# Performance work log

Hardware: AMD Instinct MI355X
Metric: run time of the kernel (lower is better)

## Reference

```python
import jax, jax.numpy as jnp
import numpy as np

NUM_EMBEDDINGS = 8192
EMBEDDING_DIM = 256
PROJECTION_DIM = 128


def setup_inputs() -> dict:
    key = jax.random.key(0)
    k_x, k_cb, k_w, k_b = jax.random.split(key, 4)
    x = jax.random.normal(k_x, (16, 1024, EMBEDDING_DIM), dtype=jnp.float32)
    codebook = jax.random.normal(k_cb, (NUM_EMBEDDINGS, EMBEDDING_DIM), dtype=jnp.float32)
    proj_w = jax.random.normal(k_w, (EMBEDDING_DIM, PROJECTION_DIM), dtype=jnp.float32) / np.sqrt(EMBEDDING_DIM)
    proj_b = jax.random.normal(k_b, (PROJECTION_DIM,), dtype=jnp.float32) * 0.01
    return {"x": x, "codebook": codebook, "proj_w": proj_w, "proj_b": proj_b}


def reference(x, codebook, proj_w, proj_b):
    # Flatten tokens: [N, D]
    x_flat = x.reshape(-1, EMBEDDING_DIM)
    # Project tokens and codebook into the distance space: [N, P], [K, P]
    x_proj = x_flat @ proj_w + proj_b
    cb_proj = codebook @ proj_w + proj_b
    # Squared euclidean distances via expansion: [N, K]
    distances = (
        jnp.sum(x_proj ** 2, axis=1, keepdims=True)
        - 2.0 * (x_proj @ cb_proj.T)
        + jnp.sum(cb_proj ** 2, axis=1)
    )
    idx = jnp.argmin(distances, axis=1)
    discrete = jax.nn.one_hot(idx, NUM_EMBEDDINGS, dtype=x.dtype)  # [N, K]
    # One-hot matmul lookup (disguised gather): [N, D]
    quantized = (discrete @ codebook).reshape(x.shape)
    return (discrete, quantized)
```

## Files before the change

kernel.cpp:

```cpp
#include <hip/hip_runtime.h>
#include <math.h>

#define D 256
#define P 128
#define K 8192
#define NTOK 16384
#define NROWS (NTOK + K)
#define NCHUNK 8
#define KCHUNK (K / NCHUNK)
#define CAPC 128
#define MARGIN 3.0f
#define FLT_BIG 3.402823466e+38f

typedef __attribute__((ext_vector_type(8))) short bf16x8;
typedef __attribute__((ext_vector_type(4))) float f32x4;
typedef __attribute__((ext_vector_type(8))) unsigned short u16x8;

__device__ __forceinline__ unsigned short f32_to_bf16_rne(float f) {
    unsigned int u = __float_as_uint(f);
    u = (u + 0x7fffu + ((u >> 16) & 1u)) >> 16;
    return (unsigned short)u;
}

__global__ __launch_bounds__(256) void proj_kernel(
    const float* __restrict__ x, const float* __restrict__ cb,
    const float* __restrict__ w, const float* __restrict__ bias,
    float* __restrict__ xproj, float* __restrict__ cproj,
    float* __restrict__ xnorm, float* __restrict__ cnorm,
    unsigned short* __restrict__ xh, unsigned short* __restrict__ chs,
    int* __restrict__ cnt)
{
    __shared__ float As[16][D];
    const int tid = threadIdx.x;
    const int row0 = blockIdx.x * 16;

    {
        int g = blockIdx.x * 256 + tid;
        if (g < NTOK) cnt[g] = 0;
    }

    for (int i = tid; i < 16 * (D / 4); i += 256) {
        int r = i / (D / 4);
        int c4 = i % (D / 4);
        int gr = row0 + r;
        const float* src = (gr < NTOK) ? (x + (size_t)gr * D)
                                       : (cb + (size_t)(gr - NTOK) * D);
        float4 v = ((const float4*)src)[c4];
        ((float4*)&As[r][0])[c4] = v;
    }
    __syncthreads();

    const int r = tid >> 4;
    const int c0 = (tid & 15) * 8;

    float acc[8];
#pragma unroll
    for (int j = 0; j < 8; j++) acc[j] = 0.f;

    for (int d = 0; d < D; d += 4) {
        float4 a4 = *(const float4*)&As[r][d];
#pragma unroll
        for (int dd = 0; dd < 4; dd++) {
            float av = (dd == 0) ? a4.x : (dd == 1) ? a4.y : (dd == 2) ? a4.z : a4.w;
            float4 w0 = *(const float4*)&w[(size_t)(d + dd) * P + c0];
            float4 w1 = *(const float4*)&w[(size_t)(d + dd) * P + c0 + 4];
            acc[0] = fmaf(av, w0.x, acc[0]);
            acc[1] = fmaf(av, w0.y, acc[1]);
            acc[2] = fmaf(av, w0.z, acc[2]);
            acc[3] = fmaf(av, w0.w, acc[3]);
            acc[4] = fmaf(av, w1.x, acc[4]);
            acc[5] = fmaf(av, w1.y, acc[5]);
            acc[6] = fmaf(av, w1.z, acc[6]);
            acc[7] = fmaf(av, w1.w, acc[7]);
        }
    }

    float out[8];
    float nrm = 0.f;
    u16x8 hv;
#pragma unroll
    for (int j = 0; j < 8; j++) {
        out[j] = acc[j] + bias[c0 + j];
        nrm = fmaf(out[j], out[j], nrm);
        hv[j] = f32_to_bf16_rne(out[j]);
    }

    const int gr = row0 + r;
    if (gr < NTOK) {
        float* dst = xproj + (size_t)gr * P;
        float4 o0; o0.x = out[0]; o0.y = out[1]; o0.z = out[2]; o0.w = out[3];
        float4 o1; o1.x = out[4]; o1.y = out[5]; o1.z = out[6]; o1.w = out[7];
        *(float4*)&dst[c0] = o0;
        *(float4*)&dst[c0 + 4] = o1;
        *(u16x8*)(xh + (size_t)gr * P + c0) = hv;
    } else {
        int row = gr - NTOK;
        float* dst = cproj + (size_t)row * P;
        float4 o0; o0.x = out[0]; o0.y = out[1]; o0.z = out[2]; o0.w = out[3];
        float4 o1; o1.x = out[4]; o1.y = out[5]; o1.z = out[6]; o1.w = out[7];
        *(float4*)&dst[c0] = o0;
        *(float4*)&dst[c0 + 4] = o1;
        int t64 = row >> 6, rg = (row >> 4) & 3, l15 = row & 15;
        int ks = c0 >> 5, quad = (c0 >> 3) & 3;
        size_t atom = ((size_t)(t64 * 16 + rg * 4 + ks) * 4 + quad) * 16 + l15;
        *(u16x8*)(chs + atom * 8) = hv;
    }

#pragma unroll
    for (int off = 1; off < 16; off <<= 1)
        nrm += __shfl_xor(nrm, off, 16);
    if ((tid & 15) == 0) {
        if (gr < NTOK) xnorm[gr] = nrm;
        else           cnorm[gr - NTOK] = nrm;
    }
}

__global__ __launch_bounds__(256) void filterz_kernel(
    const unsigned short* __restrict__ xh, const unsigned short* __restrict__ chs,
    const float* __restrict__ xnorm, const float* __restrict__ cnorm,
    int* __restrict__ cnt, int* __restrict__ cand,
    float* __restrict__ discrete)
{
    const int tid = threadIdx.x;
    const int tok0 = blockIdx.x * 128;
    const int k0 = blockIdx.y * KCHUNK;
    const int flat = blockIdx.y * gridDim.x + blockIdx.x;

    const int wave = tid >> 6;
    const int lane = tid & 63;
    const int quad = lane >> 4;
    const int l15 = lane & 15;

    f32x4* zbase = (f32x4*)discrete + (size_t)flat * 32768;
    const f32x4 zv = (f32x4)(0.f);

    bf16x8 afrag[2][4];
#pragma unroll
    for (int mi = 0; mi < 2; mi++)
#pragma unroll
        for (int ks = 0; ks < 4; ks++)
            afrag[mi][ks] = *(const bf16x8*)(
                xh + (size_t)(tok0 + wave * 32 + mi * 16 + l15) * P + ks * 32 + quad * 8);

    float xnv[2][4];
#pragma unroll
    for (int mi = 0; mi < 2; mi++)
#pragma unroll
        for (int r = 0; r < 4; r++)
            xnv[mi][r] = xnorm[tok0 + wave * 32 + mi * 16 + quad * 4 + r];

    float rmin[2][4];
#pragma unroll
    for (int mi = 0; mi < 2; mi++)
#pragma unroll
        for (int r = 0; r < 4; r++) rmin[mi][r] = FLT_BIG;

    for (int ct = 0; ct < KCHUNK / 64; ct++) {
        const int kt = k0 + ct * 64;
        const int t64 = kt >> 6;

#pragma unroll
        for (int s = 0; s < 8; s++)
            zbase[(size_t)ct * 2048 + s * 256 + tid] = zv;

        f32x4 acc[2][4];
#pragma unroll
        for (int mi = 0; mi < 2; mi++)
#pragma unroll
            for (int nj = 0; nj < 4; nj++)
                acc[mi][nj] = (f32x4)(0.f);

#pragma unroll
        for (int ks = 0; ks < 4; ks++) {
            const bf16x8* base = (const bf16x8*)(chs) + (size_t)(t64 * 16 + ks) * 64 + lane;
            bf16x8 b0 = base[0 * 4 * 64];
            bf16x8 b1 = base[1 * 4 * 64];
            bf16x8 b2 = base[2 * 4 * 64];
            bf16x8 b3 = base[3 * 4 * 64];
            acc[0][0] = __builtin_amdgcn_mfma_f32_16x16x32_bf16(afrag[0][ks], b0, acc[0][0], 0, 0, 0);
            acc[0][1] = __builtin_amdgcn_mfma_f32_16x16x32_bf16(afrag[0][ks], b1, acc[0][1], 0, 0, 0);
            acc[0][2] = __builtin_amdgcn_mfma_f32_16x16x32_bf16(afrag[0][ks], b2, acc[0][2], 0, 0, 0);
            acc[0][3] = __builtin_amdgcn_mfma_f32_16x16x32_bf16(afrag[0][ks], b3, acc[0][3], 0, 0, 0);
            acc[1][0] = __builtin_amdgcn_mfma_f32_16x16x32_bf16(afrag[1][ks], b0, acc[1][0], 0, 0, 0);
            acc[1][1] = __builtin_amdgcn_mfma_f32_16x16x32_bf16(afrag[1][ks], b1, acc[1][1], 0, 0, 0);
            acc[1][2] = __builtin_amdgcn_mfma_f32_16x16x32_bf16(afrag[1][ks], b2, acc[1][2], 0, 0, 0);
            acc[1][3] = __builtin_amdgcn_mfma_f32_16x16x32_bf16(afrag[1][ks], b3, acc[1][3], 0, 0, 0);
        }

        float cn[4];
#pragma unroll
        for (int nj = 0; nj < 4; nj++) cn[nj] = cnorm[kt + nj * 16 + l15];

#pragma unroll
        for (int mi = 0; mi < 2; mi++)
#pragma unroll
            for (int r = 0; r < 4; r++) {
                float d[4];
#pragma unroll
                for (int nj = 0; nj < 4; nj++)
                    d[nj] = (xnv[mi][r] - 2.0f * acc[mi][nj][r]) + cn[nj];
                float m = fminf(fminf(d[0], d[1]), fminf(d[2], d[3]));
#pragma unroll
                for (int off = 1; off < 16; off <<= 1)
                    m = fminf(m, __shfl_xor(m, off));
                float rm = fminf(rmin[mi][r], m);
                rmin[mi][r] = rm;
                float thr = rm + MARGIN;
                const int tok = tok0 + wave * 32 + mi * 16 + quad * 4 + r;
#pragma unroll
                for (int nj = 0; nj < 4; nj++) {
                    if (d[nj] <= thr) {
                        int pos = atomicAdd(&cnt[tok], 1);
                        if (pos < CAPC) cand[(size_t)tok * CAPC + pos] = kt + nj * 16 + l15;
                    }
                }
            }
    }
}

__global__ __launch_bounds__(256) void rescorefinal_kernel(
    const float* __restrict__ xproj, const float* __restrict__ cproj,
    const float* __restrict__ xnorm, const float* __restrict__ cnorm,
    const int* __restrict__ cnt, const int* __restrict__ cand,
    const float* __restrict__ cb,
    float* __restrict__ discrete, float* __restrict__ quant)
{
    __shared__ int sidx[64];
    const int tid = threadIdx.x;
    const int lane = tid & 63;
    const int wave = tid >> 6;
    const int tok0 = blockIdx.x * 64;

    for (int i = 0; i < 16; i++) {
        const int t = tok0 + wave * 16 + i;
        int n = cnt[t];
        if (n > CAPC) n = CAPC;
        const float xn = xnorm[t];
        const float* xr = xproj + (size_t)t * P;

        unsigned long long pack = 0xFFFFFFFFFFFFFFFFull;
        for (int j = lane; j < n; j += 64) {
            int k = cand[(size_t)t * CAPC + j];
            const float* cr = cproj + (size_t)k * P;
            float s = 0.f;
#pragma unroll 8
            for (int p = 0; p < P; p += 4) {
                float4 a = *(const float4*)&xr[p];
                float4 b = *(const float4*)&cr[p];
                s = fmaf(a.x, b.x, s);
                s = fmaf(a.y, b.y, s);
                s = fmaf(a.z, b.z, s);
                s = fmaf(a.w, b.w, s);
            }
            float dist = (xn - 2.0f * s) + cnorm[k];
            unsigned long long pk =
                ((unsigned long long)__float_as_uint(dist) << 32) |
                (unsigned long long)(unsigned)k;
            if (pk < pack) pack = pk;
        }
#pragma unroll
        for (int off = 1; off < 64; off <<= 1) {
            unsigned long long o = __shfl_xor((long long)pack, off);
            if (o < pack) pack = o;
        }
        if (lane == 0) {
            int bi = (int)(pack & 0xFFFFFFFFull);
            sidx[wave * 16 + i] = bi;
            discrete[(size_t)t * K + bi] = 1.0f;
        }
    }
    __syncthreads();

    for (int i = tid; i < 64 * (D / 4); i += 256) {
        int t = i >> 6;
        int c4 = i & 63;
        int bi = sidx[t];
        float4 v = ((const float4*)(cb + (size_t)bi * D))[c4];
        ((float4*)(quant + (size_t)(tok0 + t) * D))[c4] = v;
    }
}

extern "C" void kernel_launch(void* const* d_in, const int* in_sizes, int n_in,
                              void* d_out, int out_size, void* d_ws, size_t ws_size,
                              hipStream_t stream) {
    const float* x    = (const float*)d_in[0];
    const float* cb   = (const float*)d_in[1];
    const float* w    = (const float*)d_in[2];
    const float* bias = (const float*)d_in[3];

    float* out = (float*)d_out;
    float* discrete = out;
    float* quant = out + (size_t)NTOK * K;

    char* ws = (char*)d_ws;
    size_t off = 0;
    float* xproj = (float*)(ws + off); off += (size_t)NTOK * P * 4;
    float* cproj = (float*)(ws + off); off += (size_t)K * P * 4;
    float* xnorm = (float*)(ws + off); off += (size_t)NTOK * 4;
    float* cnorm = (float*)(ws + off); off += (size_t)K * 4;
    unsigned short* xh  = (unsigned short*)(ws + off); off += (size_t)NTOK * P * 2;
    unsigned short* chs = (unsigned short*)(ws + off); off += (size_t)K * P * 2;
    int* cnt  = (int*)(ws + off); off += (size_t)NTOK * 4;
    int* cand = (int*)(ws + off); off += (size_t)NTOK * CAPC * 4;

    proj_kernel<<<dim3(NROWS / 16), dim3(256), 0, stream>>>(
        x, cb, w, bias, xproj, cproj, xnorm, cnorm, xh, chs, cnt);

    filterz_kernel<<<dim3(NTOK / 128, NCHUNK), dim3(256), 0, stream>>>(
        xh, chs, xnorm, cnorm, cnt, cand, discrete);

    rescorefinal_kernel<<<dim3(NTOK / 64), dim3(256), 0, stream>>>(
        xproj, cproj, xnorm, cnorm, cnt, cand, cb, discrete, quant);
}
```

Before: 895.5 us.

## Fuse projection, filter and rescore into one cooperative persistent kernel

Merges the three kernels into a single cooperative kernel of 512 blocks that uses grid-wide syncs between the projection, the candidate filter and the rescore/gather phases. Zeroing of the large one-hot output moves to the start of the kernel as a grid-stride loop, so it is no longer interleaved with the MFMA filter. The filter is re-tiled so each block handles 64 tokens over half the codebook, and the candidate cap is halved. This removes launch gaps and lets the zero-fill overlap other work, but caps parallelism at 512 blocks, adds grid-sync cost, and risks overflowing the smaller candidate list.

```diff
diff --git a/kernel.cpp b/kernel.cpp
--- a/kernel.cpp
+++ b/kernel.cpp
@@ -1,4 +1,5 @@
 #include <hip/hip_runtime.h>
+#include <hip/hip_cooperative_groups.h>
 #include <math.h>
 
 #define D 256
@@ -6,11 +7,10 @@
 #define K 8192
 #define NTOK 16384
 #define NROWS (NTOK + K)
-#define NCHUNK 8
-#define KCHUNK (K / NCHUNK)
-#define CAPC 128
+#define CAPC 64
 #define MARGIN 3.0f
 #define FLT_BIG 3.402823466e+38f
+#define GRID 512
 
 typedef __attribute__((ext_vector_type(8))) short bf16x8;
 typedef __attribute__((ext_vector_type(4))) float f32x4;
@@ -22,191 +22,175 @@
     return (unsigned short)u;
 }
 
-__global__ __launch_bounds__(256) void proj_kernel(
+__global__ __launch_bounds__(256, 2) void mega_kernel(
     const float* __restrict__ x, const float* __restrict__ cb,
     const float* __restrict__ w, const float* __restrict__ bias,
     float* __restrict__ xproj, float* __restrict__ cproj,
     float* __restrict__ xnorm, float* __restrict__ cnorm,
     unsigned short* __restrict__ xh, unsigned short* __restrict__ chs,
-    int* __restrict__ cnt)
+    int* __restrict__ cnt, int* __restrict__ cand,
+    float* __restrict__ discrete, float* __restrict__ quant)
 {
+    cooperative_groups::grid_group grid = cooperative_groups::this_grid();
+
     __shared__ float As[16][D];
+    __shared__ int sidx[32];
+
     const int tid = threadIdx.x;
-    const int row0 = blockIdx.x * 16;
+    const int bid = blockIdx.x;
+    const int lane = tid & 63;
+    const int wave = tid >> 6;
+    const int quad = lane >> 4;
+    const int l15 = lane & 15;
 
     {
-        int g = blockIdx.x * 256 + tid;
+        f32x4* p = (f32x4*)discrete;
+        const f32x4 zv = (f32x4)(0.f);
+        size_t i = (size_t)bid * 256 + tid;
+        const size_t n4 = (size_t)NTOK * K / 4;
+        for (; i < n4; i += (size_t)GRID * 256) p[i] = zv;
+        int g = bid * 256 + tid;
         if (g < NTOK) cnt[g] = 0;
     }
 
-    for (int i = tid; i < 16 * (D / 4); i += 256) {
-        int r = i / (D / 4);
-        int c4 = i % (D / 4);
-        int gr = row0 + r;
-        const float* src = (gr < NTOK) ? (x + (size_t)gr * D)
-                                       : (cb + (size_t)(gr - NTOK) * D);
-        float4 v = ((const float4*)src)[c4];
-        ((float4*)&As[r][0])[c4] = v;
-    }
-    __syncthreads();
-
-    const int r = tid >> 4;
-    const int c0 = (tid & 15) * 8;
-
-    float acc[8];
-#pragma unroll
-    for (int j = 0; j < 8; j++) acc[j] = 0.f;
-
-    for (int d = 0; d < D; d += 4) {
-        float4 a4 = *(const float4*)&As[r][d];
-#pragma unroll
-        for (int dd = 0; dd < 4; dd++) {
-            float av = (dd == 0) ? a4.x : (dd == 1) ? a4.y : (dd == 2) ? a4.z : a4.w;
-            float4 w0 = *(const float4*)&w[(size_t)(d + dd) * P + c0];
-            float4 w1 = *(const float4*)&w[(size_t)(d + dd) * P + c0 + 4];
-            acc[0] = fmaf(av, w0.x, acc[0]);
-            acc[1] = fmaf(av, w0.y, acc[1]);
-            acc[2] = fmaf(av, w0.z, acc[2]);
-            acc[3] = fmaf(av, w0.w, acc[3]);
-            acc[4] = fmaf(av, w1.x, acc[4]);
-            acc[5] = fmaf(av, w1.y, acc[5]);
-            acc[6] = fmaf(av, w1.z, acc[6]);
-            acc[7] = fmaf(av, w1.w, acc[7]);
-        }
-    }
-
-    float out[8];
-    float nrm = 0.f;
-    u16x8 hv;
-#pragma unroll
-    for (int j = 0; j < 8; j++) {
-        out[j] = acc[j] + bias[c0 + j];
-        nrm = fmaf(out[j], out[j], nrm);
-        hv[j] = f32_to_bf16_rne(out[j]);
-    }
-
-    const int gr = row0 + r;
-    if (gr < NTOK) {
-        float* dst = xproj + (size_t)gr * P;
+    for (int u = bid; u < NROWS / 16; u += GRID) {
+        const int row0 = u * 16;
+        __syncthreads();
+        for (int i = tid; i < 16 * (D / 4); i += 256) {
+            int r = i / (D / 4);
+            int c4 = i % (D / 4);
+            int gr = row0 + r;
+            const float* src = (gr < NTOK) ? (x + (size_t)gr * D)
+                                           : (cb + (size_t)(gr - NTOK) * D);
+            float4 v = ((const float4*)src)[c4];
+            ((float4*)&As[r][0])[c4] = v;
+        }
+        __syncthreads();
+
+        const int r = tid >> 4;
+        const int c0 = (tid & 15) * 8;
+
+        float acc[8];
+#pragma unroll
+        for (int j = 0; j < 8; j++) acc[j] = 0.f;
+
+        for (int d = 0; d < D; d += 4) {
+            float4 a4 = *(const float4*)&As[r][d];
+#pragma unroll
+            for (int dd = 0; dd < 4; dd++) {
+                float av = (dd == 0) ? a4.x : (dd == 1) ? a4.y : (dd == 2) ? a4.z : a4.w;
+                float4 w0 = *(const float4*)&w[(size_t)(d + dd) * P + c0];
+                float4 w1 = *(const float4*)&w[(size_t)(d + dd) * P + c0 + 4];
+                acc[0] = fmaf(av, w0.x, acc[0]);
+                acc[1] = fmaf(av, w0.y, acc[1]);
+                acc[2] = fmaf(av, w0.z, acc[2]);
+                acc[3] = fmaf(av, w0.w, acc[3]);
+                acc[4] = fmaf(av, w1.x, acc[4]);
+                acc[5] = fmaf(av, w1.y, acc[5]);
+                acc[6] = fmaf(av, w1.z, acc[6]);
+                acc[7] = fmaf(av, w1.w, acc[7]);
+            }
+        }
+
+        float out[8];
+        float nrm = 0.f;
+        u16x8 hv;
+#pragma unroll
+        for (int j = 0; j < 8; j++) {
+            out[j] = acc[j] + bias[c0 + j];
+            nrm = fmaf(out[j], out[j], nrm);
+            hv[j] = f32_to_bf16_rne(out[j]);
+        }
+
+        const int gr = row0 + r;
         float4 o0; o0.x = out[0]; o0.y = out[1]; o0.z = out[2]; o0.w = out[3];
         float4 o1; o1.x = out[4]; o1.y = out[5]; o1.z = out[6]; o1.w = out[7];
-        *(float4*)&dst[c0] = o0;
-        *(float4*)&dst[c0 + 4] = o1;
-        *(u16x8*)(xh + (size_t)gr * P + c0) = hv;
-    } else {
-        int row = gr - NTOK;
-        float* dst = cproj + (size_t)row * P;
-        float4 o0; o0.x = out[0]; o0.y = out[1]; o0.z = out[2]; o0.w = out[3];
-        float4 o1; o1.x = out[4]; o1.y = out[5]; o1.z = out[6]; o1.w = out[7];
-        *(float4*)&dst[c0] = o0;
-        *(float4*)&dst[c0 + 4] = o1;
-        int t64 = row >> 6, rg = (row >> 4) & 3, l15 = row & 15;
-        int ks = c0 >> 5, quad = (c0 >> 3) & 3;
-        size_t atom = ((size_t)(t64 * 16 + rg * 4 + ks) * 4 + quad) * 16 + l15;
-        *(u16x8*)(chs + atom * 8) = hv;
-    }
-
-#pragma unroll
-    for (int off = 1; off < 16; off <<= 1)
-        nrm += __shfl_xor(nrm, off, 16);
-    if ((tid & 15) == 0) {
-        if (gr < NTOK) xnorm[gr] = nrm;
-        else           cnorm[gr - NTOK] = nrm;
-    }
-}
-
-__global__ __launch_bounds__(256) void filterz_kernel(
-    const unsigned short* __restrict__ xh, const unsigned short* __restrict__ chs,
-    const float* __restrict__ xnorm, const float* __restrict__ cnorm,
-    int* __restrict__ cnt, int* __restrict__ cand,
-    float* __restrict__ discrete)
-{
-    const int tid = threadIdx.x;
-    const int tok0 = blockIdx.x * 128;
-    const int k0 = blockIdx.y * KCHUNK;
-    const int flat = blockIdx.y * gridDim.x + blockIdx.x;
-
-    const int wave = tid >> 6;
-    const int lane = tid & 63;
-    const int quad = lane >> 4;
-    const int l15 = lane & 15;
-
-    f32x4* zbase = (f32x4*)discrete + (size_t)flat * 32768;
-    const f32x4 zv = (f32x4)(0.f);
-
-    bf16x8 afrag[2][4];
-#pragma unroll
-    for (int mi = 0; mi < 2; mi++)
+        if (gr < NTOK) {
+            float* dst = xproj + (size_t)gr * P;
+            *(float4*)&dst[c0] = o0;
+            *(float4*)&dst[c0 + 4] = o1;
+            *(u16x8*)(xh + (size_t)gr * P + c0) = hv;
+        } else {
+            int row = gr - NTOK;
+            float* dst = cproj + (size_t)row * P;
+            *(float4*)&dst[c0] = o0;
+            *(float4*)&dst[c0 + 4] = o1;
+            int t64 = row >> 6, rg = (row >> 4) & 3, rl = row & 15;
+            int ks = c0 >> 5, q = (c0 >> 3) & 3;
+            size_t atom = ((size_t)(t64 * 16 + rg * 4 + ks) * 4 + q) * 16 + rl;
+            *(u16x8*)(chs + atom * 8) = hv;
+        }
+
+#pragma unroll
+        for (int off = 1; off < 16; off <<= 1)
+            nrm += __shfl_xor(nrm, off, 16);
+        if ((tid & 15) == 0) {
+            if (gr < NTOK) xnorm[gr] = nrm;
+            else           cnorm[gr - NTOK] = nrm;
+        }
+    }
+
+    grid.sync();
+
+    {
+        const int g = bid >> 1;
+        const int h = bid & 1;
+        const int tok0 = g * 64;
+        const int trow = tok0 + wave * 16;
+
+        bf16x8 afrag[4];
 #pragma unroll
         for (int ks = 0; ks < 4; ks++)
-            afrag[mi][ks] = *(const bf16x8*)(
-                xh + (size_t)(tok0 + wave * 32 + mi * 16 + l15) * P + ks * 32 + quad * 8);
-
-    float xnv[2][4];
-#pragma unroll
-    for (int mi = 0; mi < 2; mi++)
+            afrag[ks] = *(const bf16x8*)(xh + (size_t)(trow + l15) * P + ks * 32 + quad * 8);
+
+        float xnv[4];
 #pragma unroll
         for (int r = 0; r < 4; r++)
-            xnv[mi][r] = xnorm[tok0 + wave * 32 + mi * 16 + quad * 4 + r];
-
-    float rmin[2][4];
-#pragma unroll
-    for (int mi = 0; mi < 2; mi++)
-#pragma unroll
-        for (int r = 0; r < 4; r++) rmin[mi][r] = FLT_BIG;
-
-    for (int ct = 0; ct < KCHUNK / 64; ct++) {
-        const int kt = k0 + ct * 64;
-        const int t64 = kt >> 6;
-
-#pragma unroll
-        for (int s = 0; s < 8; s++)
-            zbase[(size_t)ct * 2048 + s * 256 + tid] = zv;
-
-        f32x4 acc[2][4];
-#pragma unroll
-        for (int mi = 0; mi < 2; mi++)
-#pragma unroll
-            for (int nj = 0; nj < 4; nj++)
-                acc[mi][nj] = (f32x4)(0.f);
-
-#pragma unroll
-        for (int ks = 0; ks < 4; ks++) {
-            const bf16x8* base = (const bf16x8*)(chs) + (size_t)(t64 * 16 + ks) * 64 + lane;
-            bf16x8 b0 = base[0 * 4 * 64];
-            bf16x8 b1 = base[1 * 4 * 64];
-            bf16x8 b2 = base[2 * 4 * 64];
-            bf16x8 b3 = base[3 * 4 * 64];
-            acc[0][0] = __builtin_amdgcn_mfma_f32_16x16x32_bf16(afrag[0][ks], b0, acc[0][0], 0, 0, 0);
-            acc[0][1] = __builtin_amdgcn_mfma_f32_16x16x32_bf16(afrag[0][ks], b1, acc[0][1], 0, 0, 0);
-            acc[0][2] = __builtin_amdgcn_mfma_f32_16x16x32_bf16(afrag[0][ks], b2, acc[0][2], 0, 0, 0);
-            acc[0][3] = __builtin_amdgcn_mfma_f32_16x16x32_bf16(afrag[0][ks], b3, acc[0][3], 0, 0, 0);
-            acc[1][0] = __builtin_amdgcn_mfma_f32_16x16x32_bf16(afrag[1][ks], b0, acc[1][0], 0, 0, 0);
-            acc[1][1] = __builtin_amdgcn_mfma_f32_16x16x32_bf16(afrag[1][ks], b1, acc[1][1], 0, 0, 0);
-            acc[1][2] = __builtin_amdgcn_mfma_f32_16x16x32_bf16(afrag[1][ks], b2, acc[1][2], 0, 0, 0);
-            acc[1][3] = __builtin_amdgcn_mfma_f32_16x16x32_bf16(afrag[1][ks], b3, acc[1][3], 0, 0, 0);
-        }
-
-        float cn[4];
-#pragma unroll
-        for (int nj = 0; nj < 4; nj++) cn[nj] = cnorm[kt + nj * 16 + l15];
-
-#pragma unroll
-        for (int mi = 0; mi < 2; mi++)
+            xnv[r] = xnorm[trow + quad * 4 + r];
+
+        float rmin[4];
+#pragma unroll
+        for (int r = 0; r < 4; r++) rmin[r] = FLT_BIG;
+
+        for (int ct = 0; ct < 64; ct++) {
+            const int kt = h * 4096 + ct * 64;
+            const int t64 = kt >> 6;
+
+            f32x4 acc[4];
+#pragma unroll
+            for (int nj = 0; nj < 4; nj++) acc[nj] = (f32x4)(0.f);
+
+#pragma unroll
+            for (int ks = 0; ks < 4; ks++) {
+                const bf16x8* base = (const bf16x8*)(chs) + (size_t)(t64 * 16 + ks) * 64 + lane;
+                bf16x8 b0 = base[0 * 4 * 64];
+                bf16x8 b1 = base[1 * 4 * 64];
+                bf16x8 b2 = base[2 * 4 * 64];
+                bf16x8 b3 = base[3 * 4 * 64];
+                acc[0] = __builtin_amdgcn_mfma_f32_16x16x32_bf16(afrag[ks], b0, acc[0], 0, 0, 0);
+                acc[1] = __builtin_amdgcn_mfma_f32_16x16x32_bf16(afrag[ks], b1, acc[1], 0, 0, 0);
+                acc[2] = __builtin_amdgcn_mfma_f32_16x16x32_bf16(afrag[ks], b2, acc[2], 0, 0, 0);
+                acc[3] = __builtin_amdgcn_mfma_f32_16x16x32_bf16(afrag[ks], b3, acc[3], 0, 0, 0);
+            }
+
+            float cn[4];
+#pragma unroll
+            for (int nj = 0; nj < 4; nj++) cn[nj] = cnorm[kt + nj * 16 + l15];
+
 #pragma unroll
             for (int r = 0; r < 4; r++) {
                 float d[4];
 #pragma unroll
                 for (int nj = 0; nj < 4; nj++)
-                    d[nj] = (xnv[mi][r] - 2.0f * acc[mi][nj][r]) + cn[nj];
+                    d[nj] = (xnv[r] - 2.0f * acc[nj][r]) + cn[nj];
                 float m = fminf(fminf(d[0], d[1]), fminf(d[2], d[3]));
 #pragma unroll
                 for (int off = 1; off < 16; off <<= 1)
                     m = fminf(m, __shfl_xor(m, off));
-                float rm = fminf(rmin[mi][r], m);
-                rmin[mi][r] = rm;
+                float rm = fminf(rmin[r], m);
+                rmin[r] = rm;
                 float thr = rm + MARGIN;
-                const int tok = tok0 + wave * 32 + mi * 16 + quad * 4 + r;
+                const int tok = trow + quad * 4 + r;
 #pragma unroll
                 for (int nj = 0; nj < 4; nj++) {
                     if (d[nj] <= thr) {
@@ -215,68 +199,60 @@
                     }
                 }
             }
-    }
-}
-
-__global__ __launch_bounds__(256) void rescorefinal_kernel(
-    const float* __restrict__ xproj, const float* __restrict__ cproj,
-    const float* __restrict__ xnorm, const float* __restrict__ cnorm,
-    const int* __restrict__ cnt, const int* __restrict__ cand,
-    const float* __restrict__ cb,
-    float* __restrict__ discrete, float* __restrict__ quant)
-{
-    __shared__ int sidx[64];
-    const int tid = threadIdx.x;
-    const int lane = tid & 63;
-    const int wave = tid >> 6;
-    const int tok0 = blockIdx.x * 64;
-
-    for (int i = 0; i < 16; i++) {
-        const int t = tok0 + wave * 16 + i;
-        int n = cnt[t];
-        if (n > CAPC) n = CAPC;
-        const float xn = xnorm[t];
-        const float* xr = xproj + (size_t)t * P;
-
-        unsigned long long pack = 0xFFFFFFFFFFFFFFFFull;
-        for (int j = lane; j < n; j += 64) {
-            int k = cand[(size_t)t * CAPC + j];
-            const float* cr = cproj + (size_t)k * P;
-            float s = 0.f;
+        }
+    }
+
+    grid.sync();
+
+    {
+        const int tok0 = bid * 32;
+        for (int i = 0; i < 8; i++) {
+            const int t = tok0 + wave * 8 + i;
+            int n = cnt[t];
+            if (n > CAPC) n = CAPC;
+            const float xn = xnorm[t];
+            const float* xr = xproj + (size_t)t * P;
+
+            unsigned long long pack = 0xFFFFFFFFFFFFFFFFull;
+            for (int j = lane; j < n; j += 64) {
+                int k = cand[(size_t)t * CAPC + j];
+                const float* cr = cproj + (size_t)k * P;
+                float s = 0.f;
 #pragma unroll 8
-            for (int p = 0; p < P; p += 4) {
-                float4 a = *(const float4*)&xr[p];
-                float4 b = *(const float4*)&cr[p];
-                s = fmaf(a.x, b.x, s);
-                s = fmaf(a.y, b.y, s);
-                s = fmaf(a.z, b.z, s);
-                s = fmaf(a.w, b.w, s);
-            }
-            float dist = (xn - 2.0f * s) + cnorm[k];
-            unsigned long long pk =
-                ((unsigned long long)__float_as_uint(dist) << 32) |
-                (unsigned long long)(unsigned)k;
-            if (pk < pack) pack = pk;
-        }
-#pragma unroll
-        for (int off = 1; off < 64; off <<= 1) {
-            unsigned long long o = __shfl_xor((long long)pack, off);
-            if (o < pack) pack = o;
-        }
-        if (lane == 0) {
-            int bi = (int)(pack & 0xFFFFFFFFull);
-            sidx[wave * 16 + i] = bi;
-            discrete[(size_t)t * K + bi] = 1.0f;
-        }
-    }
-    __syncthreads();
-
-    for (int i = tid; i < 64 * (D / 4); i += 256) {
-        int t = i >> 6;
-        int c4 = i & 63;
-        int bi = sidx[t];
-        float4 v = ((const float4*)(cb + (size_t)bi * D))[c4];
-        ((float4*)(quant + (size_t)(tok0 + t) * D))[c4] = v;
+                for (int p = 0; p < P; p += 4) {
+                    float4 a = *(const float4*)&xr[p];
+                    float4 b = *(const float4*)&cr[p];
+                    s = fmaf(a.x, b.x, s);
+                    s = fmaf(a.y, b.y, s);
+                    s = fmaf(a.z, b.z, s);
+                    s = fmaf(a.w, b.w, s);
+                }
+                float dist = (xn - 2.0f * s) + cnorm[k];
+                unsigned long long pk =
+                    ((unsigned long long)__float_as_uint(dist) << 32) |
+                    (unsigned long long)(unsigned)k;
+                if (pk < pack) pack = pk;
+            }
+#pragma unroll
+            for (int off = 1; off < 64; off <<= 1) {
+                unsigned long long o = __shfl_xor((long long)pack, off);
+                if (o < pack) pack = o;
+            }
+            if (lane == 0) {
+                int bi = (int)(pack & 0xFFFFFFFFull);
+                sidx[wave * 8 + i] = bi;
+                discrete[(size_t)t * K + bi] = 1.0f;
+            }
+        }
+        __syncthreads();
+
+        for (int i = tid; i < 32 * (D / 4); i += 256) {
+            int t = i >> 6;
+            int c4 = i & 63;
+            int bi = sidx[t];
+            float4 v = ((const float4*)(cb + (size_t)bi * D))[c4];
+            ((float4*)(quant + (size_t)(tok0 + t) * D))[c4] = v;
+        }
     }
 }
 
@@ -303,12 +279,12 @@
     int* cnt  = (int*)(ws + off); off += (size_t)NTOK * 4;
     int* cand = (int*)(ws + off); off += (size_t)NTOK * CAPC * 4;
 
-    proj_kernel<<<dim3(NROWS / 16), dim3(256), 0, stream>>>(
-        x, cb, w, bias, xproj, cproj, xnorm, cnorm, xh, chs, cnt);
-
-    filterz_kernel<<<dim3(NTOK / 128, NCHUNK), dim3(256), 0, stream>>>(
-        xh, chs, xnorm, cnorm, cnt, cand, discrete);
-
-    rescorefinal_kernel<<<dim3(NTOK / 64), dim3(256), 0, stream>>>(
-        xproj, cproj, xnorm, cnorm, cnt, cand, cb, discrete, quant);
+    void* args[] = {
+        (void*)&x, (void*)&cb, (void*)&w, (void*)&bias,
+        (void*)&xproj, (void*)&cproj, (void*)&xnorm, (void*)&cnorm,
+        (void*)&xh, (void*)&chs, (void*)&cnt, (void*)&cand,
+        (void*)&discrete, (void*)&quant
+    };
+    hipLaunchCooperativeKernel((void*)mega_kernel, dim3(GRID), dim3(256),
+                               args, 0, stream);
 }
```

New measurement: 998.5 us. 11.5% more time.

## Split filter into global-min pass and threshold-collect pass over codebook

Applied to the files above, without the earlier changes.

Replaces the single filter pass, which used a running per-chunk minimum, with two passes. The first computes the exact per-token global minimum distance with atomicMin while zeroing the output. The second recomputes the bf16 MFMA distances and collects only candidates within the margin of that global minimum, so far fewer atomics and candidates reach the rescore stage. The cost is doing the distance GEMM twice. It also halves the candidate capacity, changes the grid to 4 chunks of 2048 with a launch-bounds occupancy hint, and adds a bounds guard in the final kernel.

```diff
diff --git a/kernel.cpp b/kernel.cpp
--- a/kernel.cpp
+++ b/kernel.cpp
@@ -6,9 +6,7 @@
 #define K 8192
 #define NTOK 16384
 #define NROWS (NTOK + K)
-#define NCHUNK 8
-#define KCHUNK (K / NCHUNK)
-#define CAPC 128
+#define CAPC 64
 #define MARGIN 3.0f
 #define FLT_BIG 3.402823466e+38f
 
@@ -28,7 +26,7 @@
     float* __restrict__ xproj, float* __restrict__ cproj,
     float* __restrict__ xnorm, float* __restrict__ cnorm,
     unsigned short* __restrict__ xh, unsigned short* __restrict__ chs,
-    int* __restrict__ cnt)
+    int* __restrict__ cnt, int* __restrict__ gmin)
 {
     __shared__ float As[16][D];
     const int tid = threadIdx.x;
@@ -36,7 +34,7 @@
 
     {
         int g = blockIdx.x * 256 + tid;
-        if (g < NTOK) cnt[g] = 0;
+        if (g < NTOK) { cnt[g] = 0; gmin[g] = 0x7F7FFFFF; }
     }
 
     for (int i = tid; i < 16 * (D / 4); i += 256) {
@@ -86,23 +84,21 @@
     }
 
     const int gr = row0 + r;
+    float4 o0; o0.x = out[0]; o0.y = out[1]; o0.z = out[2]; o0.w = out[3];
+    float4 o1; o1.x = out[4]; o1.y = out[5]; o1.z = out[6]; o1.w = out[7];
     if (gr < NTOK) {
         float* dst = xproj + (size_t)gr * P;
-        float4 o0; o0.x = out[0]; o0.y = out[1]; o0.z = out[2]; o0.w = out[3];
-        float4 o1; o1.x = out[4]; o1.y = out[5]; o1.z = out[6]; o1.w = out[7];
         *(float4*)&dst[c0] = o0;
         *(float4*)&dst[c0 + 4] = o1;
         *(u16x8*)(xh + (size_t)gr * P + c0) = hv;
     } else {
         int row = gr - NTOK;
         float* dst = cproj + (size_t)row * P;
-        float4 o0; o0.x = out[0]; o0.y = out[1]; o0.z = out[2]; o0.w = out[3];
-        float4 o1; o1.x = out[4]; o1.y = out[5]; o1.z = out[6]; o1.w = out[7];
         *(float4*)&dst[c0] = o0;
         *(float4*)&dst[c0 + 4] = o1;
-        int t64 = row >> 6, rg = (row >> 4) & 3, l15 = row & 15;
-        int ks = c0 >> 5, quad = (c0 >> 3) & 3;
-        size_t atom = ((size_t)(t64 * 16 + rg * 4 + ks) * 4 + quad) * 16 + l15;
+        int t64 = row >> 6, rg = (row >> 4) & 3, rl = row & 15;
+        int ks = c0 >> 5, q = (c0 >> 3) & 3;
+        size_t atom = ((size_t)(t64 * 16 + rg * 4 + ks) * 4 + q) * 16 + rl;
         *(u16x8*)(chs + atom * 8) = hv;
     }
 
@@ -115,23 +111,23 @@
     }
 }
 
-__global__ __launch_bounds__(256) void filterz_kernel(
+__global__ __launch_bounds__(256, 3) void minzero_kernel(
     const unsigned short* __restrict__ xh, const unsigned short* __restrict__ chs,
     const float* __restrict__ xnorm, const float* __restrict__ cnorm,
-    int* __restrict__ cnt, int* __restrict__ cand,
-    float* __restrict__ discrete)
+    int* __restrict__ gmin, float* __restrict__ discrete)
 {
     const int tid = threadIdx.x;
     const int tok0 = blockIdx.x * 128;
-    const int k0 = blockIdx.y * KCHUNK;
+    const int kbase = blockIdx.y * 2048;
     const int flat = blockIdx.y * gridDim.x + blockIdx.x;
 
     const int wave = tid >> 6;
     const int lane = tid & 63;
     const int quad = lane >> 4;
     const int l15 = lane & 15;
-
-    f32x4* zbase = (f32x4*)discrete + (size_t)flat * 32768;
+    const int trow = tok0 + wave * 32;
+
+    f32x4* zbase = (f32x4*)discrete + (size_t)flat * 65536;
     const f32x4 zv = (f32x4)(0.f);
 
     bf16x8 afrag[2][4];
@@ -140,14 +136,14 @@
 #pragma unroll
         for (int ks = 0; ks < 4; ks++)
             afrag[mi][ks] = *(const bf16x8*)(
-                xh + (size_t)(tok0 + wave * 32 + mi * 16 + l15) * P + ks * 32 + quad * 8);
+                xh + (size_t)(trow + mi * 16 + l15) * P + ks * 32 + quad * 8);
 
     float xnv[2][4];
 #pragma unroll
     for (int mi = 0; mi < 2; mi++)
 #pragma unroll
         for (int r = 0; r < 4; r++)
-            xnv[mi][r] = xnorm[tok0 + wave * 32 + mi * 16 + quad * 4 + r];
+            xnv[mi][r] = xnorm[trow + mi * 16 + quad * 4 + r];
 
     float rmin[2][4];
 #pragma unroll
@@ -155,8 +151,8 @@
 #pragma unroll
         for (int r = 0; r < 4; r++) rmin[mi][r] = FLT_BIG;
 
-    for (int ct = 0; ct < KCHUNK / 64; ct++) {
-        const int kt = k0 + ct * 64;
+    for (int ct = 0; ct < 32; ct++) {
+        const int kt = kbase + ct * 64;
         const int t64 = kt >> 6;
 
 #pragma unroll
@@ -167,8 +163,7 @@
 #pragma unroll
         for (int mi = 0; mi < 2; mi++)
 #pragma unroll
-            for (int nj = 0; nj < 4; nj++)
-                acc[mi][nj] = (f32x4)(0.f);
+            for (int nj = 0; nj < 4; nj++) acc[mi][nj] = (f32x4)(0.f);
 
 #pragma unroll
         for (int ks = 0; ks < 4; ks++) {
@@ -194,22 +189,101 @@
 #pragma unroll
         for (int mi = 0; mi < 2; mi++)
 #pragma unroll
+            for (int r = 0; r < 4; r++)
+#pragma unroll
+                for (int nj = 0; nj < 4; nj++) {
+                    float dd = (xnv[mi][r] - 2.0f * acc[mi][nj][r]) + cn[nj];
+                    rmin[mi][r] = fminf(rmin[mi][r], dd);
+                }
+    }
+
+#pragma unroll
+    for (int mi = 0; mi < 2; mi++)
+#pragma unroll
+        for (int r = 0; r < 4; r++) {
+            float m = rmin[mi][r];
+#pragma unroll
+            for (int off = 1; off < 16; off <<= 1)
+                m = fminf(m, __shfl_xor(m, off));
+            if (l15 == 0)
+                atomicMin(&gmin[trow + mi * 16 + quad * 4 + r], __float_as_int(m));
+        }
+}
+
+__global__ __launch_bounds__(256, 3) void collect_kernel(
+    const unsigned short* __restrict__ xh, const unsigned short* __restrict__ chs,
+    const float* __restrict__ xnorm, const float* __restrict__ cnorm,
+    const int* __restrict__ gmin,
+    int* __restrict__ cnt, int* __restrict__ cand)
+{
+    const int tid = threadIdx.x;
+    const int tok0 = blockIdx.x * 128;
+    const int kbase = blockIdx.y * 2048;
+
+    const int wave = tid >> 6;
+    const int lane = tid & 63;
+    const int quad = lane >> 4;
+    const int l15 = lane & 15;
+    const int trow = tok0 + wave * 32;
+
+    bf16x8 afrag[2][4];
+#pragma unroll
+    for (int mi = 0; mi < 2; mi++)
+#pragma unroll
+        for (int ks = 0; ks < 4; ks++)
+            afrag[mi][ks] = *(const bf16x8*)(
+                xh + (size_t)(trow + mi * 16 + l15) * P + ks * 32 + quad * 8);
+
+    float xnv[2][4], thr[2][4];
+#pragma unroll
+    for (int mi = 0; mi < 2; mi++)
+#pragma unroll
+        for (int r = 0; r < 4; r++) {
+            int t = trow + mi * 16 + quad * 4 + r;
+            xnv[mi][r] = xnorm[t];
+            thr[mi][r] = __int_as_float(gmin[t]) + MARGIN;
+        }
+
+    for (int ct = 0; ct < 32; ct++) {
+        const int kt = kbase + ct * 64;
+        const int t64 = kt >> 6;
+
+        f32x4 acc[2][4];
+#pragma unroll
+        for (int mi = 0; mi < 2; mi++)
+#pragma unroll
+            for (int nj = 0; nj < 4; nj++) acc[mi][nj] = (f32x4)(0.f);
+
+#pragma unroll
+        for (int ks = 0; ks < 4; ks++) {
+            const bf16x8* base = (const bf16x8*)(chs) + (size_t)(t64 * 16 + ks) * 64 + lane;
+            bf16x8 b0 = base[0 * 4 * 64];
+            bf16x8 b1 = base[1 * 4 * 64];
+            bf16x8 b2 = base[2 * 4 * 64];
+            bf16x8 b3 = base[3 * 4 * 64];
+            acc[0][0] = __builtin_amdgcn_mfma_f32_16x16x32_bf16(afrag[0][ks], b0, acc[0][0], 0, 0, 0);
+            acc[0][1] = __builtin_amdgcn_mfma_f32_16x16x32_bf16(afrag[0][ks], b1, acc[0][1], 0, 0, 0);
+            acc[0][2] = __builtin_amdgcn_mfma_f32_16x16x32_bf16(afrag[0][ks], b2, acc[0][2], 0, 0, 0);
+            acc[0][3] = __builtin_amdgcn_mfma_f32_16x16x32_bf16(afrag[0][ks], b3, acc[0][3], 0, 0, 0);
+            acc[1][0] = __builtin_amdgcn_mfma_f32_16x16x32_bf16(afrag[1][ks], b0, acc[1][0], 0, 0, 0);
+            acc[1][1] = __builtin_amdgcn_mfma_f32_16x16x32_bf16(afrag[1][ks], b1, acc[1][1], 0, 0, 0);
+            acc[1][2] = __builtin_amdgcn_mfma_f32_16x16x32_bf16(afrag[1][ks], b2, acc[1][2], 0, 0, 0);
+            acc[1][3] = __builtin_amdgcn_mfma_f32_16x16x32_bf16(afrag[1][ks], b3, acc[1][3], 0, 0, 0);
+        }
+
+        float cn[4];
+#pragma unroll
+        for (int nj = 0; nj < 4; nj++) cn[nj] = cnorm[kt + nj * 16 + l15];
+
+#pragma unroll
+        for (int mi = 0; mi < 2; mi++)
+#pragma unroll
             for (int r = 0; r < 4; r++) {
-                float d[4];
-#pragma unroll
-                for (int nj = 0; nj < 4; nj++)
-                    d[nj] = (xnv[mi][r] - 2.0f * acc[mi][nj][r]) + cn[nj];
-                float m = fminf(fminf(d[0], d[1]), fminf(d[2], d[3]));
-#pragma unroll
-                for (int off = 1; off < 16; off <<= 1)
-                    m = fminf(m, __shfl_xor(m, off));
-                float rm = fminf(rmin[mi][r], m);
-                rmin[mi][r] = rm;
-                float thr = rm + MARGIN;
-                const int tok = tok0 + wave * 32 + mi * 16 + quad * 4 + r;
+                const int tok = trow + mi * 16 + quad * 4 + r;
 #pragma unroll
                 for (int nj = 0; nj < 4; nj++) {
-                    if (d[nj] <= thr) {
+                    float dd = (xnv[mi][r] - 2.0f * acc[mi][nj][r]) + cn[nj];
+                    if (dd <= thr[mi][r]) {
                         int pos = atomicAdd(&cnt[tok], 1);
                         if (pos < CAPC) cand[(size_t)tok * CAPC + pos] = kt + nj * 16 + l15;
                     }
@@ -265,8 +339,10 @@
         }
         if (lane == 0) {
             int bi = (int)(pack & 0xFFFFFFFFull);
-            sidx[wave * 16 + i] = bi;
-            discrete[(size_t)t * K + bi] = 1.0f;
+            if (bi >= 0 && bi < K) {
+                sidx[wave * 16 + i] = bi;
+                discrete[(size_t)t * K + bi] = 1.0f;
+            } else sidx[wave * 16 + i] = 0;
         }
     }
     __syncthreads();
@@ -302,12 +378,16 @@
     unsigned short* chs = (unsigned short*)(ws + off); off += (size_t)K * P * 2;
     int* cnt  = (int*)(ws + off); off += (size_t)NTOK * 4;
     int* cand = (int*)(ws + off); off += (size_t)NTOK * CAPC * 4;
+    int* gmin = (int*)(ws + off); off += (size_t)NTOK * 4;
 
     proj_kernel<<<dim3(NROWS / 16), dim3(256), 0, stream>>>(
-        x, cb, w, bias, xproj, cproj, xnorm, cnorm, xh, chs, cnt);
-
-    filterz_kernel<<<dim3(NTOK / 128, NCHUNK), dim3(256), 0, stream>>>(
-        xh, chs, xnorm, cnorm, cnt, cand, discrete);
+        x, cb, w, bias, xproj, cproj, xnorm, cnorm, xh, chs, cnt, gmin);
+
+    minzero_kernel<<<dim3(NTOK / 128, 4), dim3(256), 0, stream>>>(
+        xh, chs, xnorm, cnorm, gmin, discrete);
+
+    collect_kernel<<<dim3(NTOK / 128, 4), dim3(256), 0, stream>>>(
+        xh, chs, xnorm, cnorm, gmin, cnt, cand);
 
     rescorefinal_kernel<<<dim3(NTOK / 64), dim3(256), 0, stream>>>(
         xproj, cproj, xnorm, cnorm, cnt, cand, cb, discrete, quant);
```

Measured after the change: 871.4 us. 2.7% less time.
